# Kernel tuning notes

Hardware: AMD Instinct MI355X
Metric: run time of the kernel (lower is better)

The kernel has to match this reference:

```python
import jax, jax.numpy as jnp
import numpy as np
from jax import lax

S = 512          # IMAGE_SIZE
NP = 11          # num parts (num_layers)
B = 4            # batch_size (hard-coded in original)
FEAT = 9 * 126 * 126  # fc1 in-features: 9*(((S-4)//2-2)//2)**2

_DRAW_ORDER_BIAS = [
    [0.848048096156426, -0.5299192642332049, -0.06623990802915061, 0.5299192642332049, 0.848048096156426, 0.10600601201955324],
    [0.9986295347545738, 0.05233595624294379, -0.001158806553435294, -0.05233595624294379, 0.9986295347545738, -0.022375972781727708],
    [0.8290375725550417, -0.5591929034707469, 0.2758348051438573, 0.5591929034707469, 0.8290375725550417, -0.3679706692738145],
    [0.898794046299167, -0.4383711467890774, -0.1455594743327377, 0.4383711467890774, 0.898794046299167, -0.0037996949408528533],
    [0.7431448254773944, -0.6691306063588581, -0.04191544748895007, 0.6691306063588581, 0.7431448254773944, -0.4385935274816633],
    [0.984807753012208, 0.17364817766693036, 0.09489218227886641, -0.17364817766693036, 0.984807753012208, 0.204382434413116],
    [0.754709580222772, 0.6560590289905073, 0.34755260971666235, -0.6560590289905073, 0.754709580222772, 0.3941816342013059],
    [0.992546151641322, 0.12186934340514749, 0.2294707093902736, -0.12186934340514749, 0.992546151641322, 0.42009272589950425],
    [0.766044443118978, 0.6427876096865394, 0.3722248189351549, -0.6427876096865394, 0.766044443118978, -0.02028262460152125],
    [0.9993908270190958, -0.03489949670250096, -0.16002611816129286, 0.03489949670250096, 0.9993908270190958, 0.3825967914560618],
    [0.9961946980917455, 0.08715574274765818, -0.2047079583082938, -0.08715574274765818, 0.9961946980917455, 0.15872754699051406],
]
CANON_BIAS = np.asarray(_DRAW_ORDER_BIAS, dtype=np.float32).reshape(-1)  # [66]


def setup_inputs() -> dict:
    key = jax.random.key(0)
    ks = jax.random.split(key, 8)
    x = jax.random.uniform(ks[0], (B, (NP + 1) * S, S, 4), dtype=jnp.float32)
    return {
        "x": x,
        "conv1_w": jax.random.normal(ks[1], (7, 4, 5, 5), jnp.float32) * 0.05,
        "conv1_b": jnp.zeros((7,), jnp.float32),
        "conv2_w": jax.random.normal(ks[2], (9, 7, 3, 3), jnp.float32) * 0.05,
        "conv2_b": jnp.zeros((9,), jnp.float32),
        "fc1_w": jax.random.normal(ks[3], (32, FEAT), jnp.float32) * 0.005,
        "fc1_b": jnp.zeros((32,), jnp.float32),
        "fc2_w": jax.random.normal(ks[4], (3 * NP, 32), jnp.float32) * 0.05,
        "fc2_b": jnp.zeros((3 * NP,), jnp.float32),
        "fc3_w": jax.random.normal(ks[5], (6 * NP, 3 * NP), jnp.float32) * 0.01,
        "fc3_b": jnp.asarray(CANON_BIAS),
    }


def _conv_valid(x, w, b):
    y = lax.conv_general_dilated(x, w, (1, 1), 'VALID',
                                 dimension_numbers=('NCHW', 'OIHW', 'NCHW'))
    return y + b[None, :, None, None]


def _maxpool2(x):
    return lax.reduce_window(x, -jnp.inf, lax.max, (1, 1, 2, 2), (1, 1, 2, 2), 'VALID')


def _warp(img, theta):
    """F.affine_grid + F.grid_sample (bilinear, align_corners=False, border pad).
    img: [B,C,S,S], theta: [B,2,3] -> [B,C,S,S]."""
    dt = img.dtype
    coords = (jnp.arange(S, dtype=dt) * 2 + 1) / S - 1  # align_corners=False grid
    xs = coords[None, None, :]   # [1,1,S] varies along W
    ys = coords[None, :, None]   # [1,S,1] varies along H
    gx = theta[:, 0, 0, None, None] * xs + theta[:, 0, 1, None, None] * ys + theta[:, 0, 2, None, None]
    gy = theta[:, 1, 0, None, None] * xs + theta[:, 1, 1, None, None] * ys + theta[:, 1, 2, None, None]
    # unnormalize (align_corners=False)
    ix = ((gx + 1) * S - 1) * 0.5
    iy = ((gy + 1) * S - 1) * 0.5
    x0 = jnp.floor(ix); y0 = jnp.floor(iy)
    wx = (ix - x0)[:, None]; wy = (iy - y0)[:, None]  # [B,1,S,S]
    x0i = jnp.clip(x0.astype(jnp.int32), 0, S - 1)
    x1i = jnp.clip(x0.astype(jnp.int32) + 1, 0, S - 1)
    y0i = jnp.clip(y0.astype(jnp.int32), 0, S - 1)
    y1i = jnp.clip(y0.astype(jnp.int32) + 1, 0, S - 1)
    gather = jax.vmap(lambda im, yi, xi: im[:, yi, xi])  # per-batch [C,S,S]
    v00 = gather(img, y0i, x0i); v01 = gather(img, y0i, x1i)
    v10 = gather(img, y1i, x0i); v11 = gather(img, y1i, x1i)
    return (v00 * (1 - wx) * (1 - wy) + v01 * wx * (1 - wy)
            + v10 * (1 - wx) * wy + v11 * wx * wy)


def reference(x, conv1_w, conv1_b, conv2_w, conv2_b, fc1_w, fc1_b, fc2_w, fc2_b, fc3_w, fc3_b):
    xp = x.transpose(0, 3, 1, 2)                       # [B,4,12S,S]
    chunks = xp.reshape(B, 4, NP + 1, S, S)            # split along H
    loc_in = chunks[:, :, 0]                           # [B,4,S,S]
    parts = chunks[:, :, 1:].transpose(2, 0, 1, 3, 4)  # [NP,B,4,S,S]

    # localization head
    h = _maxpool2(jax.nn.relu(_conv_valid(loc_in, conv1_w, conv1_b)))
    h = _maxpool2(jax.nn.relu(_conv_valid(h, conv2_w, conv2_b)))
    h = h.reshape(B, -1)
    h = jax.nn.relu(h @ fc1_w.T + fc1_b)
    h = jax.nn.relu(h @ fc2_w.T + fc2_b)
    theta = (h @ fc3_w.T + fc3_b).reshape(B, NP, 2, 3)  # [B,NP,2,3]

    Rm = theta[..., :2]                                 # [B,NP,2,2]
    close_to_eye = jnp.einsum('bpij,bpkj->bpik', Rm, Rm).reshape(B, NP, 4)
    translations = theta[..., 2]                        # [B,NP,2]

    warped = jax.vmap(_warp, in_axes=(0, 1))(parts, theta)  # [NP,B,4,S,S]

    stack = warped[0]
    for i in range(1, NP):
        layer = warped[i]
        alpha = jnp.clip(layer[:, -1:], 0.0, 1.0)       # [B,1,S,S]
        stack = jnp.clip(stack - 2 * alpha, -1.0, 1.0)
        stack = jnp.clip(stack + layer + 1.0, -1.0, 1.0)
    return stack, close_to_eye, translations
```

## Files before the change

kernel.cpp:

```cpp
#include <hip/hip_runtime.h>

#define SS 512
#define NPARTS 11
#define NB 4
#define FEAT (9*126*126)

#define H1SZ (4*7*254*254)
#define H2SZ (4*FEAT)
#define OFF_H1 0
#define OFF_H2 (OFF_H1 + H1SZ)
#define OFF_PART (OFF_H2 + H2SZ)
#define OFF_THETA (OFF_PART + 1024)

__global__ __launch_bounds__(256) void conv1_kernel(
    const float4* __restrict__ x4,
    const float* __restrict__ w,
    const float* __restrict__ bias,
    float* __restrict__ h1) {
  __shared__ float4 tile[36 * 37];
  int tid = threadIdx.x;
  int b = blockIdx.y;
  int by = blockIdx.x >> 4, bx = blockIdx.x & 15;
  int y0 = by * 32, x0 = bx * 32;

  const float4* img = x4 + (size_t)b * 6144 * 512;
  for (int i = tid; i < 36 * 36; i += 256) {
    int r = i / 36, c = i % 36;
    int gy = y0 + r, gx = x0 + c;
    float4 v = make_float4(0.f, 0.f, 0.f, 0.f);
    if (gy < 512 && gx < 512) v = img[(size_t)gy * 512 + gx];
    tile[r * 37 + c] = v;
  }
  __syncthreads();

  int ty = tid >> 4, tx = tid & 15;
  float acc[4][7];
#pragma unroll
  for (int p = 0; p < 4; p++)
#pragma unroll
    for (int k = 0; k < 7; k++) acc[p][k] = bias[k];

#pragma unroll
  for (int dy = 0; dy < 5; dy++) {
    const float4* r0 = &tile[(2 * ty + dy) * 37 + 2 * tx];
    const float4* r1 = r0 + 37;
    float4 a0[6], a1[6];
#pragma unroll
    for (int j = 0; j < 6; j++) { a0[j] = r0[j]; a1[j] = r1[j]; }
#pragma unroll
    for (int dx = 0; dx < 5; dx++) {
      float4 v00 = a0[dx], v01 = a0[dx + 1];
      float4 v10 = a1[dx], v11 = a1[dx + 1];
#pragma unroll
      for (int k = 0; k < 7; k++) {
        const float* wk = &w[k * 100 + dy * 5 + dx];
        float w0 = wk[0], w1 = wk[25], w2 = wk[50], w3 = wk[75];
        acc[0][k] += v00.x * w0 + v00.y * w1 + v00.z * w2 + v00.w * w3;
        acc[1][k] += v01.x * w0 + v01.y * w1 + v01.z * w2 + v01.w * w3;
        acc[2][k] += v10.x * w0 + v10.y * w1 + v10.z * w2 + v10.w * w3;
        acc[3][k] += v11.x * w0 + v11.y * w1 + v11.z * w2 + v11.w * w3;
      }
    }
  }

  int py = by * 16 + ty, px = bx * 16 + tx;
  if (py < 254 && px < 254) {
#pragma unroll
    for (int k = 0; k < 7; k++) {
      float m = fmaxf(fmaxf(acc[0][k], acc[1][k]), fmaxf(acc[2][k], acc[3][k]));
      h1[(((size_t)b * 7 + k) * 254 + py) * 254 + px] = fmaxf(m, 0.0f);
    }
  }
}

__global__ __launch_bounds__(256) void conv2_kernel(
    const float* __restrict__ h1,
    const float* __restrict__ w,
    const float* __restrict__ bias,
    float* __restrict__ h2) {
  __shared__ float tile[7 * 34 * 35];
  int tid = threadIdx.x;
  int b = blockIdx.y;
  int by = blockIdx.x >> 3, bx = blockIdx.x & 7;
  int y0 = by * 32, x0 = bx * 32;

  for (int i = tid; i < 7 * 34 * 34; i += 256) {
    int c = i / (34 * 34), rem = i % (34 * 34);
    int r = rem / 34, col = rem % 34;
    int gy = y0 + r, gx = x0 + col;
    float v = 0.f;
    if (gy < 254 && gx < 254)
      v = h1[(((size_t)b * 7 + c) * 254 + gy) * 254 + gx];
    tile[(c * 34 + r) * 35 + col] = v;
  }
  __syncthreads();

  int ty = tid >> 4, tx = tid & 15;
  float acc[4][9];
#pragma unroll
  for (int p = 0; p < 4; p++)
#pragma unroll
    for (int k = 0; k < 9; k++) acc[p][k] = bias[k];

  for (int c = 0; c < 7; c++) {
#pragma unroll
    for (int dy = 0; dy < 3; dy++) {
      const float* r0 = &tile[(c * 34 + 2 * ty + dy) * 35 + 2 * tx];
      const float* r1 = r0 + 35;
      float a0[4], a1[4];
#pragma unroll
      for (int j = 0; j < 4; j++) { a0[j] = r0[j]; a1[j] = r1[j]; }
#pragma unroll
      for (int dx = 0; dx < 3; dx++) {
#pragma unroll
        for (int k = 0; k < 9; k++) {
          float wv = w[k * 63 + c * 9 + dy * 3 + dx];
          acc[0][k] += a0[dx] * wv;
          acc[1][k] += a0[dx + 1] * wv;
          acc[2][k] += a1[dx] * wv;
          acc[3][k] += a1[dx + 1] * wv;
        }
      }
    }
  }

  int py = by * 16 + ty, px = bx * 16 + tx;
  if (py < 126 && px < 126) {
#pragma unroll
    for (int k = 0; k < 9; k++) {
      float m = fmaxf(fmaxf(acc[0][k], acc[1][k]), fmaxf(acc[2][k], acc[3][k]));
      h2[(((size_t)b * 9 + k) * 126 + py) * 126 + px] = fmaxf(m, 0.0f);
    }
  }
}

__global__ __launch_bounds__(256) void fc1_kernel(
    const float* __restrict__ h2,
    const float* __restrict__ w,
    float* __restrict__ partials) {
  int j = blockIdx.x;
  int s = blockIdx.y;
  int tid = threadIdx.x;
  const int CH = (FEAT + 7) / 8;
  int f0 = s * CH;
  int f1 = f0 + CH; if (f1 > FEAT) f1 = FEAT;
  float a0 = 0.f, a1 = 0.f, a2 = 0.f, a3 = 0.f;
  const float* wj = w + (size_t)j * FEAT;
  for (int f = f0 + tid; f < f1; f += 256) {
    float wv = wj[f];
    a0 += wv * h2[f];
    a1 += wv * h2[FEAT + f];
    a2 += wv * h2[2 * FEAT + f];
    a3 += wv * h2[3 * FEAT + f];
  }
  __shared__ float4 red[256];
  red[tid] = make_float4(a0, a1, a2, a3);
  __syncthreads();
  for (int off = 128; off > 0; off >>= 1) {
    if (tid < off) {
      float4 o = red[tid + off];
      red[tid].x += o.x; red[tid].y += o.y; red[tid].z += o.z; red[tid].w += o.w;
    }
    __syncthreads();
  }
  if (tid == 0) {
    float4 r = red[0];
    float* p = partials + ((size_t)j * 8 + s) * 4;
    p[0] = r.x; p[1] = r.y; p[2] = r.z; p[3] = r.w;
  }
}

__global__ __launch_bounds__(256) void head_kernel(
    const float* __restrict__ partials,
    const float* __restrict__ b1,
    const float* __restrict__ w2,
    const float* __restrict__ b2,
    const float* __restrict__ w3,
    const float* __restrict__ b3,
    float* __restrict__ theta_out,
    float* __restrict__ out_tail) {
  __shared__ float h32[128];
  __shared__ float h33[132];
  __shared__ float th[264];
  int tid = threadIdx.x;
  for (int t = tid; t < 128; t += 256) {
    int b = t >> 5, j = t & 31;
    float sacc = b1[j];
    for (int k = 0; k < 8; k++) sacc += partials[((size_t)j * 8 + k) * 4 + b];
    h32[b * 32 + j] = fmaxf(sacc, 0.0f);
  }
  __syncthreads();
  for (int t = tid; t < 132; t += 256) {
    int b = t / 33, j2 = t % 33;
    float sacc = b2[j2];
    for (int j = 0; j < 32; j++) sacc += h32[b * 32 + j] * w2[j2 * 32 + j];
    h33[b * 33 + j2] = fmaxf(sacc, 0.0f);
  }
  __syncthreads();
  for (int t = tid; t < 264; t += 256) {
    int b = t / 66, u = t % 66;
    float sacc = b3[u];
    for (int j2 = 0; j2 < 33; j2++) sacc += h33[b * 33 + j2] * w3[u * 33 + j2];
    th[t] = sacc;
    theta_out[t] = sacc;
  }
  __syncthreads();
  for (int t = tid; t < 176; t += 256) {
    int b = t / 44, r = t % 44, p = r / 4, ik = r % 4;
    int i = ik >> 1, k = ik & 1;
    const float* T = &th[b * 66 + p * 6];
    out_tail[t] = T[i * 3 + 0] * T[k * 3 + 0] + T[i * 3 + 1] * T[k * 3 + 1];
  }
  for (int t = tid; t < 88; t += 256) {
    int b = t / 22, r = t % 22, p = r / 2, i = r % 2;
    out_tail[176 + t] = th[b * 66 + p * 6 + i * 3 + 2];
  }
}

__global__ __launch_bounds__(256) void warp_kernel(
    const float4* __restrict__ x4,
    const float* __restrict__ theta,
    float* __restrict__ out) {
  int bid = blockIdx.x;
  int swz = (bid & 7) * 512 + (bid >> 3);
  int b = swz >> 10;
  int t = swz & 1023;
  int ty = t >> 5, tx = t & 31;
  int tid = threadIdx.x;
  int wv = tid >> 6, l = tid & 63;
  int y = ty * 16 + wv * 4 + (l >> 4);
  int x = tx * 16 + (l & 15);

  __shared__ float th[66];
  if (tid < 66) th[tid] = theta[b * 66 + tid];
  __syncthreads();

  const float4* img0 = x4 + (size_t)b * 6144 * 512;
  float fx = (float)x, fy = (float)y;
  float4 stack = make_float4(0.f, 0.f, 0.f, 0.f);
  const float c0 = (1.0f / 512.0f) - 1.0f;
#pragma unroll 1
  for (int i = 0; i < NPARTS; i++) {
    float T0 = th[i * 6 + 0], T1 = th[i * 6 + 1], T2 = th[i * 6 + 2];
    float T3 = th[i * 6 + 3], T4 = th[i * 6 + 4], T5 = th[i * 6 + 5];
    float Cx = 256.0f * ((T0 + T1) * c0 + T2) + 255.5f;
    float Cy = 256.0f * ((T3 + T4) * c0 + T5) + 255.5f;
    float ix = T0 * fx + T1 * fy + Cx;
    float iy = T3 * fx + T4 * fy + Cy;
    float x0 = floorf(ix), y0 = floorf(iy);
    float wx = ix - x0, wy = iy - y0;
    int x0i = min(max((int)x0, 0), 511);
    int x1i = min(max((int)x0 + 1, 0), 511);
    int y0i = min(max((int)y0, 0), 511);
    int y1i = min(max((int)y0 + 1, 0), 511);
    const float4* img = img0 + (size_t)(i + 1) * 512 * 512;
    float4 v00 = img[y0i * 512 + x0i];
    float4 v01 = img[y0i * 512 + x1i];
    float4 v10 = img[y1i * 512 + x0i];
    float4 v11 = img[y1i * 512 + x1i];
    float w00 = (1.f - wx) * (1.f - wy), w01 = wx * (1.f - wy);
    float w10 = (1.f - wx) * wy, w11 = wx * wy;
    float4 val;
    val.x = v00.x * w00 + v01.x * w01 + v10.x * w10 + v11.x * w11;
    val.y = v00.y * w00 + v01.y * w01 + v10.y * w10 + v11.y * w11;
    val.z = v00.z * w00 + v01.z * w01 + v10.z * w10 + v11.z * w11;
    val.w = v00.w * w00 + v01.w * w01 + v10.w * w10 + v11.w * w11;
    if (i == 0) {
      stack = val;
    } else {
      float a = fminf(fmaxf(val.w, 0.0f), 1.0f);
      stack.x = fminf(fmaxf(stack.x - 2.f * a, -1.f), 1.f);
      stack.y = fminf(fmaxf(stack.y - 2.f * a, -1.f), 1.f);
      stack.z = fminf(fmaxf(stack.z - 2.f * a, -1.f), 1.f);
      stack.w = fminf(fmaxf(stack.w - 2.f * a, -1.f), 1.f);
      stack.x = fminf(fmaxf(stack.x + val.x + 1.f, -1.f), 1.f);
      stack.y = fminf(fmaxf(stack.y + val.y + 1.f, -1.f), 1.f);
      stack.z = fminf(fmaxf(stack.z + val.z + 1.f, -1.f), 1.f);
      stack.w = fminf(fmaxf(stack.w + val.w + 1.f, -1.f), 1.f);
    }
  }
  size_t obase = (size_t)b * 4 * 262144 + (size_t)y * 512 + x;
  out[obase] = stack.x;
  out[obase + 262144] = stack.y;
  out[obase + 2 * 262144] = stack.z;
  out[obase + 3 * 262144] = stack.w;
}

extern "C" void kernel_launch(void* const* d_in, const int* in_sizes, int n_in,
                              void* d_out, int out_size, void* d_ws, size_t ws_size,
                              hipStream_t stream) {
  const float4* x4 = (const float4*)d_in[0];
  const float* conv1_w = (const float*)d_in[1];
  const float* conv1_b = (const float*)d_in[2];
  const float* conv2_w = (const float*)d_in[3];
  const float* conv2_b = (const float*)d_in[4];
  const float* fc1_w = (const float*)d_in[5];
  const float* fc1_b = (const float*)d_in[6];
  const float* fc2_w = (const float*)d_in[7];
  const float* fc2_b = (const float*)d_in[8];
  const float* fc3_w = (const float*)d_in[9];
  const float* fc3_b = (const float*)d_in[10];
  float* ws = (float*)d_ws;
  float* out = (float*)d_out;

  conv1_kernel<<<dim3(256, 4), 256, 0, stream>>>(x4, conv1_w, conv1_b, ws + OFF_H1);
  conv2_kernel<<<dim3(64, 4), 256, 0, stream>>>(ws + OFF_H1, conv2_w, conv2_b, ws + OFF_H2);
  fc1_kernel<<<dim3(32, 8), 256, 0, stream>>>(ws + OFF_H2, fc1_w, ws + OFF_PART);
  head_kernel<<<1, 256, 0, stream>>>(ws + OFF_PART, fc1_b, fc2_w, fc2_b, fc3_w, fc3_b,
                                     ws + OFF_THETA, out + 4194304);
  warp_kernel<<<4096, 256, 0, stream>>>(x4, ws + OFF_THETA, out);
}
```

Before: 139.1 us.

## Stage warp source footprint in LDS with 32x32 output tiles per block

The warp kernel now processes a 32x32 output tile per block, with four pixels per thread. For each part it computes the bounding box of the source footprint and, when that box fits in 48x48, cooperatively loads it into swizzled shared memory. The bilinear taps are then read from shared memory instead of global memory. This aims to cut redundant gather traffic, at the cost of extra barriers, an unused-texel load overhead, a fallback path for large footprints, and fewer blocks.

```diff
diff --git a/kernel.cpp b/kernel.cpp
--- a/kernel.cpp
+++ b/kernel.cpp
@@ -221,69 +221,112 @@
     const float4* __restrict__ x4,
     const float* __restrict__ theta,
     float* __restrict__ out) {
+  __shared__ float4 tile[48 * 48];
+  __shared__ float th[66];
   int bid = blockIdx.x;
-  int swz = (bid & 7) * 512 + (bid >> 3);
-  int b = swz >> 10;
-  int t = swz & 1023;
-  int ty = t >> 5, tx = t & 31;
-  int tid = threadIdx.x;
-  int wv = tid >> 6, l = tid & 63;
-  int y = ty * 16 + wv * 4 + (l >> 4);
-  int x = tx * 16 + (l & 15);
-
-  __shared__ float th[66];
+  int swz = (bid & 7) * 128 + (bid >> 3);
+  int b = swz >> 8;
+  int t = swz & 255;
+  int ty0 = (t >> 4) * 32, tx0 = (t & 15) * 32;
+  int tid = threadIdx.x;
   if (tid < 66) th[tid] = theta[b * 66 + tid];
   __syncthreads();
 
+  int r0 = tid >> 5, c0 = tid & 31;
   const float4* img0 = x4 + (size_t)b * 6144 * 512;
-  float fx = (float)x, fy = (float)y;
-  float4 stack = make_float4(0.f, 0.f, 0.f, 0.f);
-  const float c0 = (1.0f / 512.0f) - 1.0f;
+  const float cn = (1.0f / 512.0f) - 1.0f;
+  float4 stack[4];
+
 #pragma unroll 1
   for (int i = 0; i < NPARTS; i++) {
     float T0 = th[i * 6 + 0], T1 = th[i * 6 + 1], T2 = th[i * 6 + 2];
     float T3 = th[i * 6 + 3], T4 = th[i * 6 + 4], T5 = th[i * 6 + 5];
-    float Cx = 256.0f * ((T0 + T1) * c0 + T2) + 255.5f;
-    float Cy = 256.0f * ((T3 + T4) * c0 + T5) + 255.5f;
-    float ix = T0 * fx + T1 * fy + Cx;
-    float iy = T3 * fx + T4 * fy + Cy;
-    float x0 = floorf(ix), y0 = floorf(iy);
-    float wx = ix - x0, wy = iy - y0;
-    int x0i = min(max((int)x0, 0), 511);
-    int x1i = min(max((int)x0 + 1, 0), 511);
-    int y0i = min(max((int)y0, 0), 511);
-    int y1i = min(max((int)y0 + 1, 0), 511);
-    const float4* img = img0 + (size_t)(i + 1) * 512 * 512;
-    float4 v00 = img[y0i * 512 + x0i];
-    float4 v01 = img[y0i * 512 + x1i];
-    float4 v10 = img[y1i * 512 + x0i];
-    float4 v11 = img[y1i * 512 + x1i];
-    float w00 = (1.f - wx) * (1.f - wy), w01 = wx * (1.f - wy);
-    float w10 = (1.f - wx) * wy, w11 = wx * wy;
-    float4 val;
-    val.x = v00.x * w00 + v01.x * w01 + v10.x * w10 + v11.x * w11;
-    val.y = v00.y * w00 + v01.y * w01 + v10.y * w10 + v11.y * w11;
-    val.z = v00.z * w00 + v01.z * w01 + v10.z * w10 + v11.z * w11;
-    val.w = v00.w * w00 + v01.w * w01 + v10.w * w10 + v11.w * w11;
-    if (i == 0) {
-      stack = val;
-    } else {
-      float a = fminf(fmaxf(val.w, 0.0f), 1.0f);
-      stack.x = fminf(fmaxf(stack.x - 2.f * a, -1.f), 1.f);
-      stack.y = fminf(fmaxf(stack.y - 2.f * a, -1.f), 1.f);
-      stack.z = fminf(fmaxf(stack.z - 2.f * a, -1.f), 1.f);
-      stack.w = fminf(fmaxf(stack.w - 2.f * a, -1.f), 1.f);
-      stack.x = fminf(fmaxf(stack.x + val.x + 1.f, -1.f), 1.f);
-      stack.y = fminf(fmaxf(stack.y + val.y + 1.f, -1.f), 1.f);
-      stack.z = fminf(fmaxf(stack.z + val.z + 1.f, -1.f), 1.f);
-      stack.w = fminf(fmaxf(stack.w + val.w + 1.f, -1.f), 1.f);
-    }
-  }
-  size_t obase = (size_t)b * 4 * 262144 + (size_t)y * 512 + x;
-  out[obase] = stack.x;
-  out[obase + 262144] = stack.y;
-  out[obase + 2 * 262144] = stack.z;
-  out[obase + 3 * 262144] = stack.w;
+    float Cx = 256.0f * ((T0 + T1) * cn + T2) + 255.5f;
+    float Cy = 256.0f * ((T3 + T4) * cn + T5) + 255.5f;
+    float xa = T0 * (float)tx0, xb = T0 * (float)(tx0 + 31);
+    float ya = T1 * (float)ty0, yb = T1 * (float)(ty0 + 31);
+    float ixmin = fminf(xa, xb) + fminf(ya, yb) + Cx;
+    float ixmax = fmaxf(xa, xb) + fmaxf(ya, yb) + Cx;
+    xa = T3 * (float)tx0; xb = T3 * (float)(tx0 + 31);
+    ya = T4 * (float)ty0; yb = T4 * (float)(ty0 + 31);
+    float iymin = fminf(xa, xb) + fminf(ya, yb) + Cy;
+    float iymax = fmaxf(xa, xb) + fmaxf(ya, yb) + Cy;
+    int sx0 = min(max((int)floorf(ixmin), 0), 511);
+    int sx1 = min(max((int)floorf(ixmax) + 1, 0), 511);
+    int sy0 = min(max((int)floorf(iymin), 0), 511);
+    int sy1 = min(max((int)floorf(iymax) + 1, 0), 511);
+    int W = sx1 - sx0 + 1, H = sy1 - sy0 + 1;
+    const float4* img = img0 + (size_t)(i + 1) * 262144;
+    bool use_lds = (W <= 48) && (H <= 48);
+
+    if (i) __syncthreads();
+    if (use_lds) {
+      int n = W * H;
+      for (int k = tid; k < n; k += 256) {
+        int rr = k / W, cc = k - rr * W;
+        tile[rr * 48 + (cc ^ (rr & 7))] = img[(size_t)(sy0 + rr) * 512 + (sx0 + cc)];
+      }
+    }
+    __syncthreads();
+
+#pragma unroll
+    for (int k = 0; k < 4; k++) {
+      float fx = (float)(tx0 + c0), fy = (float)(ty0 + r0 + 8 * k);
+      float ix = T0 * fx + T1 * fy + Cx;
+      float iy = T3 * fx + T4 * fy + Cy;
+      float xf = floorf(ix), yf = floorf(iy);
+      float wx = ix - xf, wy = iy - yf;
+      int x0i = min(max((int)xf, 0), 511);
+      int x1i = min(max((int)xf + 1, 0), 511);
+      int y0i = min(max((int)yf, 0), 511);
+      int y1i = min(max((int)yf + 1, 0), 511);
+      float4 v00, v01, v10, v11;
+      if (use_lds) {
+        int lx0 = x0i - sx0, lx1 = x1i - sx0;
+        int ly0 = y0i - sy0, ly1 = y1i - sy0;
+        int e0 = ly0 & 7, e1 = ly1 & 7;
+        v00 = tile[ly0 * 48 + (lx0 ^ e0)];
+        v01 = tile[ly0 * 48 + (lx1 ^ e0)];
+        v10 = tile[ly1 * 48 + (lx0 ^ e1)];
+        v11 = tile[ly1 * 48 + (lx1 ^ e1)];
+      } else {
+        v00 = img[y0i * 512 + x0i];
+        v01 = img[y0i * 512 + x1i];
+        v10 = img[y1i * 512 + x0i];
+        v11 = img[y1i * 512 + x1i];
+      }
+      float w00 = (1.f - wx) * (1.f - wy), w01 = wx * (1.f - wy);
+      float w10 = (1.f - wx) * wy, w11 = wx * wy;
+      float4 val;
+      val.x = v00.x * w00 + v01.x * w01 + v10.x * w10 + v11.x * w11;
+      val.y = v00.y * w00 + v01.y * w01 + v10.y * w10 + v11.y * w11;
+      val.z = v00.z * w00 + v01.z * w01 + v10.z * w10 + v11.z * w11;
+      val.w = v00.w * w00 + v01.w * w01 + v10.w * w10 + v11.w * w11;
+      if (i == 0) {
+        stack[k] = val;
+      } else {
+        float a = fminf(fmaxf(val.w, 0.0f), 1.0f);
+        stack[k].x = fminf(fmaxf(stack[k].x - 2.f * a, -1.f), 1.f);
+        stack[k].y = fminf(fmaxf(stack[k].y - 2.f * a, -1.f), 1.f);
+        stack[k].z = fminf(fmaxf(stack[k].z - 2.f * a, -1.f), 1.f);
+        stack[k].w = fminf(fmaxf(stack[k].w - 2.f * a, -1.f), 1.f);
+        stack[k].x = fminf(fmaxf(stack[k].x + val.x + 1.f, -1.f), 1.f);
+        stack[k].y = fminf(fmaxf(stack[k].y + val.y + 1.f, -1.f), 1.f);
+        stack[k].z = fminf(fmaxf(stack[k].z + val.z + 1.f, -1.f), 1.f);
+        stack[k].w = fminf(fmaxf(stack[k].w + val.w + 1.f, -1.f), 1.f);
+      }
+    }
+  }
+
+#pragma unroll
+  for (int k = 0; k < 4; k++) {
+    int y = ty0 + r0 + 8 * k, x = tx0 + c0;
+    size_t obase = (size_t)b * 4 * 262144 + (size_t)y * 512 + x;
+    out[obase] = stack[k].x;
+    out[obase + 262144] = stack[k].y;
+    out[obase + 2 * 262144] = stack[k].z;
+    out[obase + 3 * 262144] = stack[k].w;
+  }
 }
 
 extern "C" void kernel_launch(void* const* d_in, const int* in_sizes, int n_in,
@@ -308,5 +351,5 @@
   fc1_kernel<<<dim3(32, 8), 256, 0, stream>>>(ws + OFF_H2, fc1_w, ws + OFF_PART);
   head_kernel<<<1, 256, 0, stream>>>(ws + OFF_PART, fc1_b, fc2_w, fc2_b, fc3_w, fc3_b,
                                      ws + OFF_THETA, out + 4194304);
-  warp_kernel<<<4096, 256, 0, stream>>>(x4, ws + OFF_THETA, out);
-}
+  warp_kernel<<<1024, 256, 0, stream>>>(x4, ws + OFF_THETA, out);
+}
```

Result: slower. 161.1 us (+15.8%).

## Convert part planes to fp16 in a pre-pass and gather halves in warp

Applied to the files above, without the earlier changes.

Adds a conversion kernel that rewrites the 11 part planes of each batch item into packed fp16 in workspace. The warp kernel then fetches each bilinear row pair with a single 16-byte load of two adjacent half4 texels instead of four float4 gathers. The aim is to halve the bytes the gather-heavy warp kernel reads. In exchange it adds a full extra read of the fp32 planes plus an fp16 write on every call, and it loses input precision.

```diff
diff --git a/kernel.cpp b/kernel.cpp
--- a/kernel.cpp
+++ b/kernel.cpp
@@ -1,4 +1,5 @@
 #include <hip/hip_runtime.h>
+#include <hip/hip_fp16.h>
 
 #define SS 512
 #define NPARTS 11
@@ -11,6 +12,31 @@
 #define OFF_H2 (OFF_H1 + H1SZ)
 #define OFF_PART (OFF_H2 + H2SZ)
 #define OFF_THETA (OFF_PART + 1024)
+#define OFF_HALF (OFF_THETA + 264)
+
+__device__ inline float2 h2f(unsigned u) {
+  __half2 h = *reinterpret_cast<__half2*>(&u);
+  return __half22float2(h);
+}
+
+__global__ __launch_bounds__(256) void tohalf_kernel(
+    const float4* __restrict__ x4, uint2* __restrict__ hw) {
+  int b = blockIdx.y;
+  const float4* src = x4 + (size_t)b * 6144 * 512 + 262144;
+  uint2* dst = hw + (size_t)b * 11 * 262144;
+  int base = blockIdx.x * 2048 + threadIdx.x;
+#pragma unroll
+  for (int j = 0; j < 8; j++) {
+    int idx = base + j * 256;
+    float4 v = src[idx];
+    __half2 h01 = __float22half2_rn(make_float2(v.x, v.y));
+    __half2 h23 = __float22half2_rn(make_float2(v.z, v.w));
+    uint2 o;
+    o.x = *reinterpret_cast<unsigned*>(&h01);
+    o.y = *reinterpret_cast<unsigned*>(&h23);
+    dst[idx] = o;
+  }
+}
 
 __global__ __launch_bounds__(256) void conv1_kernel(
     const float4* __restrict__ x4,
@@ -218,7 +244,7 @@
 }
 
 __global__ __launch_bounds__(256) void warp_kernel(
-    const float4* __restrict__ x4,
+    const uint2* __restrict__ hw,
     const float* __restrict__ theta,
     float* __restrict__ out) {
   int bid = blockIdx.x;
@@ -235,36 +261,46 @@
   if (tid < 66) th[tid] = theta[b * 66 + tid];
   __syncthreads();
 
-  const float4* img0 = x4 + (size_t)b * 6144 * 512;
   float fx = (float)x, fy = (float)y;
+  const float cn = (1.0f / 512.0f) - 1.0f;
+  const uint2* plane0 = hw + (size_t)b * 11 * 262144;
+
   float4 stack = make_float4(0.f, 0.f, 0.f, 0.f);
-  const float c0 = (1.0f / 512.0f) - 1.0f;
 #pragma unroll 1
   for (int i = 0; i < NPARTS; i++) {
     float T0 = th[i * 6 + 0], T1 = th[i * 6 + 1], T2 = th[i * 6 + 2];
     float T3 = th[i * 6 + 3], T4 = th[i * 6 + 4], T5 = th[i * 6 + 5];
-    float Cx = 256.0f * ((T0 + T1) * c0 + T2) + 255.5f;
-    float Cy = 256.0f * ((T3 + T4) * c0 + T5) + 255.5f;
-    float ix = T0 * fx + T1 * fy + Cx;
-    float iy = T3 * fx + T4 * fy + Cy;
-    float x0 = floorf(ix), y0 = floorf(iy);
-    float wx = ix - x0, wy = iy - y0;
-    int x0i = min(max((int)x0, 0), 511);
-    int x1i = min(max((int)x0 + 1, 0), 511);
-    int y0i = min(max((int)y0, 0), 511);
-    int y1i = min(max((int)y0 + 1, 0), 511);
-    const float4* img = img0 + (size_t)(i + 1) * 512 * 512;
-    float4 v00 = img[y0i * 512 + x0i];
-    float4 v01 = img[y0i * 512 + x1i];
-    float4 v10 = img[y1i * 512 + x0i];
-    float4 v11 = img[y1i * 512 + x1i];
+    float Cx = 256.0f * ((T0 + T1) * cn + T2) + 255.5f;
+    float Cy = 256.0f * ((T3 + T4) * cn + T5) + 255.5f;
+    float ix = fmaf(T0, fx, fmaf(T1, fy, Cx));
+    float iy = fmaf(T3, fx, fmaf(T4, fy, Cy));
+    float xf = floorf(ix), yf = floorf(iy);
+    float wx = ix - xf, wy = iy - yf;
+    int x0 = (int)xf;
+    int x0i = min(max(x0, 0), 511);
+    int x1i = min(max(x0 + 1, 0), 511);
+    int y0i = min(max((int)yf, 0), 511);
+    int y1i = min(max((int)yf + 1, 0), 511);
+    int xbase = min(max(x0, 0), 510);
+    const uint2* plane = plane0 + (size_t)i * 262144;
+    uint4 r0 = *reinterpret_cast<const uint4*>(plane + y0i * 512 + xbase);
+    uint4 r1 = *reinterpret_cast<const uint4*>(plane + y1i * 512 + xbase);
+    bool s0 = x0i > xbase, s1 = x1i > xbase;
+    unsigned u00a = s0 ? r0.z : r0.x, u00b = s0 ? r0.w : r0.y;
+    unsigned u01a = s1 ? r0.z : r0.x, u01b = s1 ? r0.w : r0.y;
+    unsigned u10a = s0 ? r1.z : r1.x, u10b = s0 ? r1.w : r1.y;
+    unsigned u11a = s1 ? r1.z : r1.x, u11b = s1 ? r1.w : r1.y;
+    float2 p00a = h2f(u00a), p00b = h2f(u00b);
+    float2 p01a = h2f(u01a), p01b = h2f(u01b);
+    float2 p10a = h2f(u10a), p10b = h2f(u10b);
+    float2 p11a = h2f(u11a), p11b = h2f(u11b);
     float w00 = (1.f - wx) * (1.f - wy), w01 = wx * (1.f - wy);
     float w10 = (1.f - wx) * wy, w11 = wx * wy;
     float4 val;
-    val.x = v00.x * w00 + v01.x * w01 + v10.x * w10 + v11.x * w11;
-    val.y = v00.y * w00 + v01.y * w01 + v10.y * w10 + v11.y * w11;
-    val.z = v00.z * w00 + v01.z * w01 + v10.z * w10 + v11.z * w11;
-    val.w = v00.w * w00 + v01.w * w01 + v10.w * w10 + v11.w * w11;
+    val.x = p00a.x * w00 + p01a.x * w01 + p10a.x * w10 + p11a.x * w11;
+    val.y = p00a.y * w00 + p01a.y * w01 + p10a.y * w10 + p11a.y * w11;
+    val.z = p00b.x * w00 + p01b.x * w01 + p10b.x * w10 + p11b.x * w11;
+    val.w = p00b.y * w00 + p01b.y * w01 + p10b.y * w10 + p11b.y * w11;
     if (i == 0) {
       stack = val;
     } else {
@@ -302,11 +338,13 @@
   const float* fc3_b = (const float*)d_in[10];
   float* ws = (float*)d_ws;
   float* out = (float*)d_out;
-
+  uint2* hw = (uint2*)(ws + OFF_HALF);
+
+  tohalf_kernel<<<dim3(1408, 4), 256, 0, stream>>>(x4, hw);
   conv1_kernel<<<dim3(256, 4), 256, 0, stream>>>(x4, conv1_w, conv1_b, ws + OFF_H1);
   conv2_kernel<<<dim3(64, 4), 256, 0, stream>>>(ws + OFF_H1, conv2_w, conv2_b, ws + OFF_H2);
   fc1_kernel<<<dim3(32, 8), 256, 0, stream>>>(ws + OFF_H2, fc1_w, ws + OFF_PART);
   head_kernel<<<1, 256, 0, stream>>>(ws + OFF_PART, fc1_b, fc2_w, fc2_b, fc3_w, fc3_b,
                                      ws + OFF_THETA, out + 4194304);
-  warp_kernel<<<4096, 256, 0, stream>>>(x4, ws + OFF_THETA, out);
-}
+  warp_kernel<<<4096, 256, 0, stream>>>(hw, ws + OFF_THETA, out);
+}
```

Result: slower. 188.7 us (+35.7%).
